# Optimization experiments

Measured on AMD Instinct MI355X. Metric: run time of the kernel, lower is better.

Reference implementation:

```python
import jax, jax.numpy as jnp
import numpy as np

H = 64  # lstm hidden

def _lstm_scan(xs, h0, c0, wih, whh, bih, bhh):
    # xs: [T,B,D]; torch gate order i,f,g,o
    def step(carry, xt):
        h, c = carry
        gates = xt @ wih.T + h @ whh.T + bih + bhh
        i, f, g, o = jnp.split(gates, 4, axis=-1)
        c = jax.nn.sigmoid(f) * c + jax.nn.sigmoid(i) * jnp.tanh(g)
        h = jax.nn.sigmoid(o) * jnp.tanh(c)
        return (h, c), h
    (h, c), hs = jax.lax.scan(step, (h0, c0), xs)
    return hs, h, c


def setup_inputs() -> dict:
    key = jax.random.key(0)
    ks = jax.random.split(key, 32)
    r = lambda i, shape: (jax.random.normal(ks[i], shape, jnp.float32) * 0.05)
    B, T = 2048, 128
    inp = {
        "x": jax.random.normal(ks[0], (B, T, 37), jnp.float32),
        "enc_lin_w": r(1, (64, 37)), "enc_lin_b": r(2, (64,)),
        "enc_wih_f": r(3, (4 * H, 64)), "enc_whh_f": r(4, (4 * H, H)),
        "enc_bih_f": r(5, (4 * H,)), "enc_bhh_f": r(6, (4 * H,)),
        "enc_wih_b": r(7, (4 * H, 64)), "enc_whh_b": r(8, (4 * H, H)),
        "enc_bih_b": r(9, (4 * H,)), "enc_bhh_b": r(10, (4 * H,)),
        "att1_w": r(11, (32, 192)), "att1_b": r(12, (32,)),
        "att2_w": r(13, (1, 32)), "att2_b": r(14, (1,)),
        "dec_wih": r(15, (4 * H, 128)), "dec_whh": r(16, (4 * H, H)),
        "dec_bih": r(17, (4 * H,)), "dec_bhh": r(18, (4 * H,)),
        "dec_lin_w": r(19, (11, H)), "dec_lin_b": r(20, (11,)),
        "output_len": 10,
    }
    return inp


def reference(x, enc_lin_w, enc_lin_b,
              enc_wih_f, enc_whh_f, enc_bih_f, enc_bhh_f,
              enc_wih_b, enc_whh_b, enc_bih_b, enc_bhh_b,
              att1_w, att1_b, att2_w, att2_b,
              dec_wih, dec_whh, dec_bih, dec_bhh,
              dec_lin_w, dec_lin_b, output_len):
    B, T, _ = x.shape
    # ---- Encoder: linear -> relu -> BiLSTM ----
    e = jax.nn.relu(x @ enc_lin_w.T + enc_lin_b)          # [B,T,64]
    xs = jnp.transpose(e, (1, 0, 2))                       # [T,B,64]
    z = jnp.zeros((B, H), x.dtype)
    hf, _, _ = _lstm_scan(xs, z, z, enc_wih_f, enc_whh_f, enc_bih_f, enc_bhh_f)
    hb, _, _ = _lstm_scan(xs[::-1], z, z, enc_wih_b, enc_whh_b, enc_bih_b, enc_bhh_b)
    feats = jnp.concatenate([hf, hb[::-1]], axis=-1)       # [T,B,128]
    feats = jnp.transpose(feats, (1, 0, 2))                # [B,T,128]

    # ---- Decoder loop with (degenerate) additive attention ----
    def dec_step(carry, _):
        h, c = carry
        h_rep = jnp.broadcast_to(h[:, None, :], (B, T, H))
        fin = jnp.concatenate([feats, h_rep], axis=-1)     # [B,T,192]
        a = jnp.tanh(fin @ att1_w.T + att1_b)              # [B,T,32]
        s = a @ att2_w.T + att2_b                          # [B,T,1]
        scores = jax.nn.softmax(s, axis=-1)                # all ones (faithful to source)
        fd = jnp.sum(feats * scores, axis=1)               # [B,128]
        gates = fd @ dec_wih.T + h @ dec_whh.T + dec_bih + dec_bhh
        i, f, g, o = jnp.split(gates, 4, axis=-1)
        c = jax.nn.sigmoid(f) * c + jax.nn.sigmoid(i) * jnp.tanh(g)
        h = jax.nn.sigmoid(o) * jnp.tanh(c)
        out = jax.nn.softmax(h @ dec_lin_w.T + dec_lin_b, axis=-1)  # [B,11]
        return (h, c), out

    (_, _), outs = jax.lax.scan(dec_step, (z, z), None, length=output_len)
    return jnp.transpose(outs, (1, 0, 2))                  # [B,output_len,11]
```

## Files before the change

kernel.cpp:

```cpp
#include <hip/hip_runtime.h>


typedef _Float16 f16;
typedef f16 f16x8 __attribute__((ext_vector_type(8)));
typedef f16 f16x4 __attribute__((ext_vector_type(4)));
typedef float f32x4 __attribute__((ext_vector_type(4)));

#define MFMA16(a, b, c) __builtin_amdgcn_mfma_f32_16x16x32_f16(a, b, c, 0, 0, 0)

#define NLOG2E  -1.4426950408889634f
#define N2LOG2E -2.8853900817779268f

__device__ __forceinline__ float rcp_(float x) { return __builtin_amdgcn_rcpf(x); }
__device__ __forceinline__ float ex2_(float x) { return __builtin_amdgcn_exp2f(x); }
__device__ __forceinline__ float sigf(float x) { return 1.f / (1.f + __expf(-x)); }
__device__ __forceinline__ float tanhf_fast(float x) {
  float e = __expf(2.f * x);
  return 1.f - 2.f / (e + 1.f);
}


__global__ __launch_bounds__(256) void enc_linear_k(
    const float* __restrict__ x, const float* __restrict__ w1,
    const float* __restrict__ b1, f16* __restrict__ efrag) {
  const int bg = blockIdx.x;
  const int tc = blockIdx.y;
  const int tid = threadIdx.x;
  const int w = tid >> 6, l = tid & 63;
  const int rho = l & 15, c = l >> 4;

  __shared__ __align__(16) f16 fstage[16][2][64][8];

  f16x8 w1a[4], w1b[4];
  f32x4 ebias[4];
#pragma unroll
  for (int m = 0; m < 4; m++) {
    const float* pw = w1 + (16 * m + rho) * 37;
    f16x8 v0, v1;
#pragma unroll
    for (int i = 0; i < 8; i++) {
      v0[i] = (f16)pw[8 * c + i];
      v1[i] = (f16)((c == 0 && i < 5) ? pw[32 + i] : 0.f);
    }
    w1a[m] = v0;
    w1b[m] = v1;
#pragma unroll
    for (int r = 0; r < 4; r++) ebias[m][r] = b1[16 * m + 4 * c + r];
  }

  const float* xrow = x + (size_t)(bg * 16 + rho) * 4736 + (size_t)(tc * 16) * 37;

#pragma unroll
  for (int ti = 0; ti < 4; ti++) {
    const int tl = 4 * w + ti;
    const float* px = xrow + tl * 37;
    f16x8 xb0, xb1 = {};
#pragma unroll
    for (int i = 0; i < 8; i++) xb0[i] = (f16)px[8 * c + i];
    if (c == 0) {
#pragma unroll
      for (int i = 0; i < 5; i++) xb1[i] = (f16)px[32 + i];
    }
#pragma unroll
    for (int m = 0; m < 4; m++) {
      f32x4 ea = MFMA16(w1a[m], xb0, ebias[m]);
      ea = MFMA16(w1b[m], xb1, ea);
      f16x4 pk;
#pragma unroll
      for (int r = 0; r < 4; r++) pk[r] = (f16)fmaxf(ea[r], 0.f);
      const int d0 = 16 * m + 4 * c;
      *(f16x4*)&fstage[tl][m >> 1][rho | (((d0 >> 3) & 3) << 4)][d0 & 7] = pk;
    }
  }
  __syncthreads();

  const float4* srcf = (const float4*)fstage;
  float4* dstf = (float4*)efrag;
  for (int i = tid; i < 2048; i += 256) {
    const int tl = i >> 7, rest = i & 127;
    dstf[((size_t)((tc * 16 + tl) * 128 + bg) * 2) * 64 + rest] = srcf[i];
  }
}

__global__ __launch_bounds__(512, 2) void bilstm_k(
    const f16* __restrict__ efrag,
    const float* __restrict__ wih_f, const float* __restrict__ whh_f,
    const float* __restrict__ bih_f, const float* __restrict__ bhh_f,
    const float* __restrict__ wih_b, const float* __restrict__ whh_b,
    const float* __restrict__ bih_b, const float* __restrict__ bhh_b,
    float* __restrict__ fd) {
  const int bid = blockIdx.x;
  const int dir = bid >> 7;
  const int bg = bid & 127;
  const int tid = threadIdx.x;
  const int w = tid >> 6, l = tid & 63;
  const int rho = l & 15, c = l >> 4;
  const int gate = rho & 3, uoff = rho >> 2;

  const float* wih = dir ? wih_b : wih_f;
  const float* whh = dir ? whh_b : whh_f;
  const float* bih = dir ? bih_b : bih_f;
  const float* bhh = dir ? bhh_b : bhh_f;

  __shared__ __align__(16) f16 hbuf[2][2][64][8];
  {
    int* hz = (int*)hbuf;
    for (int i = tid; i < (int)(sizeof(hbuf) / 4); i += 512) hz[i] = 0;
  }

  const float sA = (gate == 2) ? N2LOG2E : NLOG2E;

  f16x8 aih[2][2], ahh[2][2];
#pragma unroll
  for (int q = 0; q < 2; q++) {
    const int m = 2 * w + q;
    const int n = gate * 64 + 4 * m + uoff;
#pragma unroll
    for (int ks = 0; ks < 2; ks++) {
      const float* p1 = wih + n * 64 + ks * 32 + c * 8;
      const float* p2 = whh + n * 64 + ks * 32 + c * 8;
      f16x8 v1, v2;
#pragma unroll
      for (int i = 0; i < 8; i++) {
        v1[i] = (f16)(p1[i] * sA);
        v2[i] = (f16)(p2[i] * sA);
      }
      aih[q][ks] = v1;
      ahh[q][ks] = v2;
    }
  }
  f32x4 bias[2];
#pragma unroll
  for (int q = 0; q < 2; q++) {
    const int j = 8 * w + 4 * q + c;
#pragma unroll
    for (int r = 0; r < 4; r++) {
      const float sr = (r == 2) ? N2LOG2E : NLOG2E;
      bias[q][r] = (bih[64 * r + j] + bhh[64 * r + j]) * sr;
    }
  }

  const f16x8* eb = (const f16x8*)efrag;
#define EIDX(t) (((size_t)(((dir ? 127 - (t) : (t)) * 128) + bg) * 2) * 64 + l)
  f16x8 ec0 = eb[EIDX(0)], ec1 = eb[EIDX(0) + 64];
  f16x8 e10 = eb[EIDX(1)], e11 = eb[EIDX(1) + 64];
  f16x8 e20 = eb[EIDX(2)], e21 = eb[EIDX(2) + 64];

  float cst[2] = {0.f, 0.f};
  float hs[2] = {0.f, 0.f};

  __syncthreads();

#pragma unroll 4
  for (int t = 0; t < 128; t++) {
    const int cur = t & 1;
    const int t3 = (t + 3 < 128) ? t + 3 : 127;
    const f16x8 ld0 = eb[EIDX(t3)];
    const f16x8 ld1 = eb[EIDX(t3) + 64];

    f16x8 h0 = *(const f16x8*)&hbuf[cur][0][l][0];
    f16x8 h1 = *(const f16x8*)&hbuf[cur][1][l][0];
#pragma unroll
    for (int q = 0; q < 2; q++) {
      f32x4 a = bias[q];
      a = MFMA16(aih[q][0], ec0, a);
      a = MFMA16(aih[q][1], ec1, a);
      a = MFMA16(ahh[q][0], h0, a);
      a = MFMA16(ahh[q][1], h1, a);
      const float ig = rcp_(1.f + ex2_(a[0]));
      const float fg = rcp_(1.f + ex2_(a[1]));
      const float gg = 2.f * rcp_(1.f + ex2_(a[2])) - 1.f;
      const float og = rcp_(1.f + ex2_(a[3]));
      cst[q] = fg * cst[q] + ig * gg;
      const float th = 2.f * rcp_(1.f + ex2_(cst[q] * N2LOG2E)) - 1.f;
      const float h = og * th;
      hs[q] += h;
      const int j = 8 * w + 4 * q + c;
      hbuf[cur ^ 1][j >> 5][rho | (((j >> 3) & 3) << 4)][j & 7] = (f16)h;
    }
    ec0 = e10; ec1 = e11;
    e10 = e20; e11 = e21;
    e20 = ld0; e21 = ld1;
    asm volatile("s_waitcnt lgkmcnt(0)\n\ts_barrier" ::: "memory");
  }
#undef EIDX
#pragma unroll
  for (int q = 0; q < 2; q++) {
    const int j = 8 * w + 4 * q + c;
    fd[(size_t)(bg * 16 + rho) * 128 + dir * 64 + j] = hs[q];
  }
}

__global__ __launch_bounds__(256) void decoder_k(
    const float* __restrict__ fd,
    const float* __restrict__ dwih, const float* __restrict__ dwhh,
    const float* __restrict__ dbih, const float* __restrict__ dbhh,
    const float* __restrict__ dlw, const float* __restrict__ dlb,
    const int* __restrict__ outlen_p, float* __restrict__ out) {
  const int b0 = blockIdx.x * 16;
  const int tid = threadIdx.x;
  const int w = tid >> 6, l = tid & 63;
  const int rho = l & 15, c = l >> 4;
  const int gate = rho & 3, uoff = rho >> 2;
  const int outlen = *outlen_p;

  __shared__ __align__(16) f16 hbuf[2][2][64][8];
  __shared__ float h32[64][16];
  __shared__ float ldslw[11 * 64];
  __shared__ float ldslb[16];
  __shared__ float lg[16][16];

  {
    int* hz = (int*)hbuf;
    for (int i = tid; i < (int)(sizeof(hbuf) / 4); i += 256) hz[i] = 0;
  }
  for (int i = tid; i < 704; i += 256) ldslw[i] = dlw[i];
  if (tid < 16) ldslb[tid] = (tid < 11) ? dlb[tid] : 0.f;

  f16x8 awhh[4][2];
  f32x4 acc0[4];
  {
    f16x8 bfd[4];
#pragma unroll
    for (int ks = 0; ks < 4; ks++) {
      const float* p = fd + (size_t)(b0 + rho) * 128 + ks * 32 + c * 8;
      f16x8 v;
#pragma unroll
      for (int i = 0; i < 8; i++) v[i] = (f16)p[i];
      bfd[ks] = v;
    }
#pragma unroll
    for (int q = 0; q < 4; q++) {
      const int m = 4 * w + q;
      const int n = gate * 64 + 4 * m + uoff;
      f32x4 a;
      const int j = 16 * w + 4 * q + c;
#pragma unroll
      for (int r = 0; r < 4; r++) a[r] = dbih[64 * r + j] + dbhh[64 * r + j];
#pragma unroll
      for (int ks = 0; ks < 4; ks++) {
        const float* p = dwih + n * 128 + ks * 32 + c * 8;
        f16x8 v;
#pragma unroll
        for (int i = 0; i < 8; i++) v[i] = (f16)p[i];
        a = MFMA16(v, bfd[ks], a);
      }
      acc0[q] = a;
#pragma unroll
      for (int ks = 0; ks < 2; ks++) {
        const float* p = dwhh + n * 64 + ks * 32 + c * 8;
        f16x8 v;
#pragma unroll
        for (int i = 0; i < 8; i++) v[i] = (f16)p[i];
        awhh[q][ks] = v;
      }
    }
  }
  float cst[4] = {0.f, 0.f, 0.f, 0.f};
  __syncthreads();

  for (int s = 0; s < outlen; s++) {
    const int cur = s & 1;
    f16x8 h0 = *(const f16x8*)&hbuf[cur][0][l][0];
    f16x8 h1 = *(const f16x8*)&hbuf[cur][1][l][0];
#pragma unroll
    for (int q = 0; q < 4; q++) {
      f32x4 a = acc0[q];
      a = MFMA16(awhh[q][0], h0, a);
      a = MFMA16(awhh[q][1], h1, a);
      const float ig = sigf(a[0]);
      const float fg = sigf(a[1]);
      const float gg = tanhf_fast(a[2]);
      const float og = sigf(a[3]);
      cst[q] = fg * cst[q] + ig * gg;
      const float h = og * tanhf_fast(cst[q]);
      const int j = 16 * w + 4 * q + c;
      hbuf[cur ^ 1][j >> 5][rho | (((j >> 3) & 3) << 4)][j & 7] = (f16)h;
      h32[j][rho] = h;
    }
    __syncthreads();
    const int b = tid >> 4, o = tid & 15;
    float logit = 0.f;
    if (o < 11) {
      logit = ldslb[o];
      for (int jj = 0; jj < 64; jj++) logit += h32[jj][b] * ldslw[o * 64 + jj];
      lg[b][o] = logit;
    }
    __syncthreads();
    if (o < 11) {
      float mx = lg[b][0];
      for (int k = 1; k < 11; k++) mx = fmaxf(mx, lg[b][k]);
      float sum = 0.f;
      for (int k = 0; k < 11; k++) sum += __expf(lg[b][k] - mx);
      out[(size_t)(b0 + b) * outlen * 11 + (size_t)s * 11 + o] =
          __expf(logit - mx) / sum;
    }
    __syncthreads();
  }
}

extern "C" void kernel_launch(void* const* d_in, const int* in_sizes, int n_in,
                              void* d_out, int out_size, void* d_ws, size_t ws_size,
                              hipStream_t stream) {
  const float* x = (const float*)d_in[0];
  const float* w1 = (const float*)d_in[1];
  const float* b1 = (const float*)d_in[2];
  const float* wih_f = (const float*)d_in[3];
  const float* whh_f = (const float*)d_in[4];
  const float* bih_f = (const float*)d_in[5];
  const float* bhh_f = (const float*)d_in[6];
  const float* wih_b = (const float*)d_in[7];
  const float* whh_b = (const float*)d_in[8];
  const float* bih_b = (const float*)d_in[9];
  const float* bhh_b = (const float*)d_in[10];
  const float* dwih = (const float*)d_in[15];
  const float* dwhh = (const float*)d_in[16];
  const float* dbih = (const float*)d_in[17];
  const float* dbhh = (const float*)d_in[18];
  const float* dlw = (const float*)d_in[19];
  const float* dlb = (const float*)d_in[20];
  const int* outlen = (const int*)d_in[21];
  float* out = (float*)d_out;

  f16* efrag = (f16*)d_ws;
  float* fd = (float*)((char*)d_ws + (size_t)33554432);

  hipLaunchKernelGGL(enc_linear_k, dim3(128, 8), dim3(256), 0, stream,
                     x, w1, b1, efrag);
  hipLaunchKernelGGL(bilstm_k, dim3(256), dim3(512), 0, stream,
                     efrag, wih_f, whh_f, bih_f, bhh_f,
                     wih_b, whh_b, bih_b, bhh_b, fd);
  hipLaunchKernelGGL(decoder_k, dim3(128), dim3(256), 0, stream,
                     fd, dwih, dwhh, dbih, dbhh, dlw, dlb, outlen, out);
}
```

Baseline: 118.5 us.

## Split BiLSTM recurrence across 16 waves and write encoder fragments directly

The BiLSTM kernel now launches 1024 threads per block, so each wave handles one 16-row gate tile instead of two. This halves the serial MFMA and activation chain per wave on every timestep. It also swaps the per-step index arithmetic for a pointer that moves by a fixed stride. The encoder-linear kernel drops its LDS staging and barrier and stores f16x4 fragments straight to global memory. The trade-off is a more expensive barrier across twice as many waves on each of the 128 steps, and smaller, less coalesced global stores in the encoder.

```diff
diff --git a/kernel.cpp b/kernel.cpp
--- a/kernel.cpp
+++ b/kernel.cpp
@@ -29,8 +29,6 @@
   const int w = tid >> 6, l = tid & 63;
   const int rho = l & 15, c = l >> 4;
 
-  __shared__ __align__(16) f16 fstage[16][2][64][8];
-
   f16x8 w1a[4], w1b[4];
   f32x4 ebias[4];
 #pragma unroll
@@ -61,6 +59,7 @@
 #pragma unroll
       for (int i = 0; i < 5; i++) xb1[i] = (f16)px[32 + i];
     }
+    const size_t tbase = ((size_t)((tc * 16 + tl) * 128 + bg)) * 2;
 #pragma unroll
     for (int m = 0; m < 4; m++) {
       f32x4 ea = MFMA16(w1a[m], xb0, ebias[m]);
@@ -69,20 +68,13 @@
 #pragma unroll
       for (int r = 0; r < 4; r++) pk[r] = (f16)fmaxf(ea[r], 0.f);
       const int d0 = 16 * m + 4 * c;
-      *(f16x4*)&fstage[tl][m >> 1][rho | (((d0 >> 3) & 3) << 4)][d0 & 7] = pk;
-    }
-  }
-  __syncthreads();
-
-  const float4* srcf = (const float4*)fstage;
-  float4* dstf = (float4*)efrag;
-  for (int i = tid; i < 2048; i += 256) {
-    const int tl = i >> 7, rest = i & 127;
-    dstf[((size_t)((tc * 16 + tl) * 128 + bg) * 2) * 64 + rest] = srcf[i];
-  }
-}
-
-__global__ __launch_bounds__(512, 2) void bilstm_k(
+      const int slot = rho | (((d0 >> 3) & 3) << 4);
+      *(f16x4*)&efrag[((tbase + (m >> 1)) * 64 + slot) * 8 + (d0 & 7)] = pk;
+    }
+  }
+}
+
+__global__ __launch_bounds__(1024, 4) void bilstm_k(
     const f16* __restrict__ efrag,
     const float* __restrict__ wih_f, const float* __restrict__ whh_f,
     const float* __restrict__ bih_f, const float* __restrict__ bhh_f,
@@ -103,92 +95,77 @@
   const float* bhh = dir ? bhh_b : bhh_f;
 
   __shared__ __align__(16) f16 hbuf[2][2][64][8];
-  {
-    int* hz = (int*)hbuf;
-    for (int i = tid; i < (int)(sizeof(hbuf) / 4); i += 512) hz[i] = 0;
-  }
+  ((int*)hbuf)[tid] = 0;
 
   const float sA = (gate == 2) ? N2LOG2E : NLOG2E;
 
-  f16x8 aih[2][2], ahh[2][2];
-#pragma unroll
-  for (int q = 0; q < 2; q++) {
-    const int m = 2 * w + q;
-    const int n = gate * 64 + 4 * m + uoff;
-#pragma unroll
-    for (int ks = 0; ks < 2; ks++) {
-      const float* p1 = wih + n * 64 + ks * 32 + c * 8;
-      const float* p2 = whh + n * 64 + ks * 32 + c * 8;
-      f16x8 v1, v2;
-#pragma unroll
-      for (int i = 0; i < 8; i++) {
-        v1[i] = (f16)(p1[i] * sA);
-        v2[i] = (f16)(p2[i] * sA);
-      }
-      aih[q][ks] = v1;
-      ahh[q][ks] = v2;
-    }
-  }
-  f32x4 bias[2];
-#pragma unroll
-  for (int q = 0; q < 2; q++) {
-    const int j = 8 * w + 4 * q + c;
-#pragma unroll
-    for (int r = 0; r < 4; r++) {
-      const float sr = (r == 2) ? N2LOG2E : NLOG2E;
-      bias[q][r] = (bih[64 * r + j] + bhh[64 * r + j]) * sr;
-    }
+  const int n = gate * 64 + 4 * w + uoff;
+  f16x8 aih[2], ahh[2];
+#pragma unroll
+  for (int ks = 0; ks < 2; ks++) {
+    const float* p1 = wih + n * 64 + ks * 32 + c * 8;
+    const float* p2 = whh + n * 64 + ks * 32 + c * 8;
+    f16x8 v1, v2;
+#pragma unroll
+    for (int i = 0; i < 8; i++) {
+      v1[i] = (f16)(p1[i] * sA);
+      v2[i] = (f16)(p2[i] * sA);
+    }
+    aih[ks] = v1;
+    ahh[ks] = v2;
+  }
+  const int j = 4 * w + c;
+  f32x4 bias;
+#pragma unroll
+  for (int r = 0; r < 4; r++) {
+    const float sr = (r == 2) ? N2LOG2E : NLOG2E;
+    bias[r] = (bih[64 * r + j] + bhh[64 * r + j]) * sr;
   }
 
   const f16x8* eb = (const f16x8*)efrag;
-#define EIDX(t) (((size_t)(((dir ? 127 - (t) : (t)) * 128) + bg) * 2) * 64 + l)
-  f16x8 ec0 = eb[EIDX(0)], ec1 = eb[EIDX(0) + 64];
-  f16x8 e10 = eb[EIDX(1)], e11 = eb[EIDX(1) + 64];
-  f16x8 e20 = eb[EIDX(2)], e21 = eb[EIDX(2) + 64];
-
-  float cst[2] = {0.f, 0.f};
-  float hs[2] = {0.f, 0.f};
+  const ptrdiff_t dstep = dir ? -(ptrdiff_t)16384 : (ptrdiff_t)16384;
+  const f16x8* p0 = eb + (((size_t)((dir ? 127 : 0) * 128 + bg)) * 2) * 64 + l;
+  f16x8 ec0 = p0[0], ec1 = p0[64];
+  f16x8 e10 = p0[dstep], e11 = p0[dstep + 64];
+  f16x8 e20 = p0[2 * dstep], e21 = p0[2 * dstep + 64];
+  const f16x8* p3 = p0 + 3 * dstep;
+
+  float cst = 0.f, hs = 0.f;
 
   __syncthreads();
 
+  const int hslot = rho | (((j >> 3) & 3) << 4);
 #pragma unroll 4
   for (int t = 0; t < 128; t++) {
     const int cur = t & 1;
-    const int t3 = (t + 3 < 128) ? t + 3 : 127;
-    const f16x8 ld0 = eb[EIDX(t3)];
-    const f16x8 ld1 = eb[EIDX(t3) + 64];
-
-    f16x8 h0 = *(const f16x8*)&hbuf[cur][0][l][0];
-    f16x8 h1 = *(const f16x8*)&hbuf[cur][1][l][0];
-#pragma unroll
-    for (int q = 0; q < 2; q++) {
-      f32x4 a = bias[q];
-      a = MFMA16(aih[q][0], ec0, a);
-      a = MFMA16(aih[q][1], ec1, a);
-      a = MFMA16(ahh[q][0], h0, a);
-      a = MFMA16(ahh[q][1], h1, a);
-      const float ig = rcp_(1.f + ex2_(a[0]));
-      const float fg = rcp_(1.f + ex2_(a[1]));
-      const float gg = 2.f * rcp_(1.f + ex2_(a[2])) - 1.f;
-      const float og = rcp_(1.f + ex2_(a[3]));
-      cst[q] = fg * cst[q] + ig * gg;
-      const float th = 2.f * rcp_(1.f + ex2_(cst[q] * N2LOG2E)) - 1.f;
-      const float h = og * th;
-      hs[q] += h;
-      const int j = 8 * w + 4 * q + c;
-      hbuf[cur ^ 1][j >> 5][rho | (((j >> 3) & 3) << 4)][j & 7] = (f16)h;
-    }
+    const f16x8 ld0 = p3[0];
+    const f16x8 ld1 = p3[64];
+    if (t < 124) p3 += dstep;
+
+    const f16x8 h0 = *(const f16x8*)&hbuf[cur][0][l][0];
+    const f16x8 h1 = *(const f16x8*)&hbuf[cur][1][l][0];
+    f32x4 a = bias;
+    a = MFMA16(aih[0], ec0, a);
+    a = MFMA16(aih[1], ec1, a);
+    a = MFMA16(ahh[0], h0, a);
+    a = MFMA16(ahh[1], h1, a);
+    const float ig = rcp_(1.f + ex2_(a[0]));
+    const float fg = rcp_(1.f + ex2_(a[1]));
+    const float gg = 2.f * rcp_(1.f + ex2_(a[2])) - 1.f;
+    const float og = rcp_(1.f + ex2_(a[3]));
+    cst = fg * cst + ig * gg;
+    const float th = 2.f * rcp_(1.f + ex2_(cst * N2LOG2E)) - 1.f;
+    const float h = og * th;
+    hs += h;
+    hbuf[cur ^ 1][j >> 5][hslot][j & 7] = (f16)h;
+
     ec0 = e10; ec1 = e11;
     e10 = e20; e11 = e21;
     e20 = ld0; e21 = ld1;
     asm volatile("s_waitcnt lgkmcnt(0)\n\ts_barrier" ::: "memory");
   }
-#undef EIDX
-#pragma unroll
-  for (int q = 0; q < 2; q++) {
-    const int j = 8 * w + 4 * q + c;
-    fd[(size_t)(bg * 16 + rho) * 128 + dir * 64 + j] = hs[q];
-  }
+
+  fd[(size_t)(bg * 16 + rho) * 128 + dir * 64 + j] = hs;
 }
 
 __global__ __launch_bounds__(256) void decoder_k(
@@ -327,7 +304,7 @@
 
   hipLaunchKernelGGL(enc_linear_k, dim3(128, 8), dim3(256), 0, stream,
                      x, w1, b1, efrag);
-  hipLaunchKernelGGL(bilstm_k, dim3(256), dim3(512), 0, stream,
+  hipLaunchKernelGGL(bilstm_k, dim3(256), dim3(1024), 0, stream,
                      efrag, wih_f, whh_f, bih_f, bhh_f,
                      wih_b, whh_b, bih_b, bhh_b, fd);
   hipLaunchKernelGGL(decoder_k, dim3(128), dim3(256), 0, stream,
```

Measured after the change: 119.8 us. No clear change (+1.1%).

## Stage x in LDS with coalesced loads and write linear layout directly

Applied to the files above, without the earlier changes.

The encoder linear kernel now copies each block's x tile into shared memory with float4 loads before building MFMA operands, rather than doing strided scalar global reads. It writes results straight to a simpler [t][b][row][64] f16 layout, which removes the LDS staging buffer and the repack copy. The grid doubles to 16 time-chunks of 8 steps each. The BiLSTM kernel's indexing is changed to read the new layout. The cost is that BiLSTM fragment loads are no longer contiguous 64-lane float4 runs, which may affect the recurrent kernel's load pattern.

```diff
diff --git a/kernel.cpp b/kernel.cpp
--- a/kernel.cpp
+++ b/kernel.cpp
@@ -19,17 +19,27 @@
   return 1.f - 2.f / (e + 1.f);
 }
 
-
+#define XSTRIDE 300
 __global__ __launch_bounds__(256) void enc_linear_k(
     const float* __restrict__ x, const float* __restrict__ w1,
-    const float* __restrict__ b1, f16* __restrict__ efrag) {
+    const float* __restrict__ b1, f16* __restrict__ elin) {
   const int bg = blockIdx.x;
   const int tc = blockIdx.y;
   const int tid = threadIdx.x;
   const int w = tid >> 6, l = tid & 63;
   const int rho = l & 15, c = l >> 4;
 
-  __shared__ __align__(16) f16 fstage[16][2][64][8];
+  __shared__ float xls[16 * XSTRIDE];
+
+  {
+    const float* xbase = x + (size_t)(bg * 16) * 4736 + tc * 296;
+    for (int cidx = tid; cidx < 16 * 74; cidx += 256) {
+      const int r = cidx / 74;
+      const int f = cidx - r * 74;
+      const float4 v = *(const float4*)(xbase + (size_t)r * 4736 + 4 * f);
+      *(float4*)&xls[r * XSTRIDE + 4 * f] = v;
+    }
+  }
 
   f16x8 w1a[4], w1b[4];
   f32x4 ebias[4];
@@ -47,13 +57,12 @@
 #pragma unroll
     for (int r = 0; r < 4; r++) ebias[m][r] = b1[16 * m + 4 * c + r];
   }
-
-  const float* xrow = x + (size_t)(bg * 16 + rho) * 4736 + (size_t)(tc * 16) * 37;
-
-#pragma unroll
-  for (int ti = 0; ti < 4; ti++) {
-    const int tl = 4 * w + ti;
-    const float* px = xrow + tl * 37;
+  __syncthreads();
+
+#pragma unroll
+  for (int ti = 0; ti < 2; ti++) {
+    const int tl = 2 * w + ti;
+    const float* px = xls + rho * XSTRIDE + tl * 37;
     f16x8 xb0, xb1 = {};
 #pragma unroll
     for (int i = 0; i < 8; i++) xb0[i] = (f16)px[8 * c + i];
@@ -61,6 +70,8 @@
 #pragma unroll
       for (int i = 0; i < 5; i++) xb1[i] = (f16)px[32 + i];
     }
+    const size_t obase =
+        (((size_t)(tc * 8 + tl) * 128 + bg) * 16 + rho) * 64;
 #pragma unroll
     for (int m = 0; m < 4; m++) {
       f32x4 ea = MFMA16(w1a[m], xb0, ebias[m]);
@@ -68,22 +79,13 @@
       f16x4 pk;
 #pragma unroll
       for (int r = 0; r < 4; r++) pk[r] = (f16)fmaxf(ea[r], 0.f);
-      const int d0 = 16 * m + 4 * c;
-      *(f16x4*)&fstage[tl][m >> 1][rho | (((d0 >> 3) & 3) << 4)][d0 & 7] = pk;
-    }
-  }
-  __syncthreads();
-
-  const float4* srcf = (const float4*)fstage;
-  float4* dstf = (float4*)efrag;
-  for (int i = tid; i < 2048; i += 256) {
-    const int tl = i >> 7, rest = i & 127;
-    dstf[((size_t)((tc * 16 + tl) * 128 + bg) * 2) * 64 + rest] = srcf[i];
+      *(f16x4*)&elin[obase + 16 * m + 4 * c] = pk;
+    }
   }
 }
 
 __global__ __launch_bounds__(512, 2) void bilstm_k(
-    const f16* __restrict__ efrag,
+    const f16* __restrict__ elin,
     const float* __restrict__ wih_f, const float* __restrict__ whh_f,
     const float* __restrict__ bih_f, const float* __restrict__ bhh_f,
     const float* __restrict__ wih_b, const float* __restrict__ whh_b,
@@ -140,11 +142,11 @@
     }
   }
 
-  const f16x8* eb = (const f16x8*)efrag;
-#define EIDX(t) (((size_t)(((dir ? 127 - (t) : (t)) * 128) + bg) * 2) * 64 + l)
-  f16x8 ec0 = eb[EIDX(0)], ec1 = eb[EIDX(0) + 64];
-  f16x8 e10 = eb[EIDX(1)], e11 = eb[EIDX(1) + 64];
-  f16x8 e20 = eb[EIDX(2)], e21 = eb[EIDX(2) + 64];
+  const f16x8* eb = (const f16x8*)elin;
+#define EIDX(t) ((((size_t)((dir ? 127 - (t) : (t)) * 128 + bg) * 16 + rho) * 8) + c)
+  f16x8 ec0 = eb[EIDX(0)], ec1 = eb[EIDX(0) + 4];
+  f16x8 e10 = eb[EIDX(1)], e11 = eb[EIDX(1) + 4];
+  f16x8 e20 = eb[EIDX(2)], e21 = eb[EIDX(2) + 4];
 
   float cst[2] = {0.f, 0.f};
   float hs[2] = {0.f, 0.f};
@@ -156,7 +158,7 @@
     const int cur = t & 1;
     const int t3 = (t + 3 < 128) ? t + 3 : 127;
     const f16x8 ld0 = eb[EIDX(t3)];
-    const f16x8 ld1 = eb[EIDX(t3) + 64];
+    const f16x8 ld1 = eb[EIDX(t3) + 4];
 
     f16x8 h0 = *(const f16x8*)&hbuf[cur][0][l][0];
     f16x8 h1 = *(const f16x8*)&hbuf[cur][1][l][0];
@@ -322,13 +324,13 @@
   const int* outlen = (const int*)d_in[21];
   float* out = (float*)d_out;
 
-  f16* efrag = (f16*)d_ws;
+  f16* elin = (f16*)d_ws;
   float* fd = (float*)((char*)d_ws + (size_t)33554432);
 
-  hipLaunchKernelGGL(enc_linear_k, dim3(128, 8), dim3(256), 0, stream,
-                     x, w1, b1, efrag);
+  hipLaunchKernelGGL(enc_linear_k, dim3(128, 16), dim3(256), 0, stream,
+                     x, w1, b1, elin);
   hipLaunchKernelGGL(bilstm_k, dim3(256), dim3(512), 0, stream,
-                     efrag, wih_f, whh_f, bih_f, bhh_f,
+                     elin, wih_f, whh_f, bih_f, bhh_f,
                      wih_b, whh_b, bih_b, bhh_b, fd);
   hipLaunchKernelGGL(decoder_k, dim3(128), dim3(256), 0, stream,
                      fd, dwih, dwhh, dbih, dbhh, dlw, dlb, outlen, out);
```

New measurement: 135.0 us. +14.0%, slower.
